# Performance work log

Hardware: AMD Instinct MI355X
Metric: run time of the kernel (lower is better)

Reference implementation:

```python
import jax, jax.numpy as jnp
import numpy as np

SDR_DIM = 65536
HIDDEN = 4096
N_MOD = 2048
PHASE = 2 * N_MOD  # 4096
NORM_EPS = 1e-8


def setup_inputs() -> dict:
    key = jax.random.key(0)
    ks = jax.random.split(key, 12)
    active_sdr = (jax.random.uniform(ks[0], (SDR_DIM,)) < 0.05).astype(jnp.float32)
    velocity = jax.random.normal(ks[1], (2,), dtype=jnp.float32)
    # encoder params (torch Linear: y = x @ W.T + b, W shape (out, in))
    W1 = jax.random.normal(ks[2], (HIDDEN, SDR_DIM), dtype=jnp.float32) * (1.0 / np.sqrt(SDR_DIM))
    b1 = jnp.zeros((HIDDEN,), dtype=jnp.float32)
    W2 = jax.random.normal(ks[3], (PHASE, HIDDEN), dtype=jnp.float32) * (1.0 / np.sqrt(HIDDEN))
    b2 = jnp.zeros((PHASE,), dtype=jnp.float32)
    # velocity encoder (no bias): (n_grid_modules, 2)
    vel_W = jax.random.normal(ks[4], (N_MOD, 2), dtype=jnp.float32) * (1.0 / np.sqrt(2.0))
    # thalamic loop: orthogonal-init square matrices, gain param, hidden state
    def ortho(k, n):
        a = jax.random.normal(k, (n, n), dtype=jnp.float32)
        q, r = jnp.linalg.qr(a)
        return q * jnp.sign(jnp.diag(r))[None, :]
    W_tc = ortho(ks[5], PHASE)
    W_ht = ortho(ks[6], PHASE)
    g_nrt = jnp.ones((PHASE,), dtype=jnp.float32)
    h_tc = jnp.zeros((PHASE,), dtype=jnp.float32)
    return {
        "active_sdr": active_sdr, "velocity": velocity,
        "W1": W1, "b1": b1, "W2": W2, "b2": b2,
        "vel_W": vel_W, "W_tc": W_tc, "W_ht": W_ht,
        "g_nrt": g_nrt, "h_tc": h_tc,
    }


def reference(active_sdr, velocity, W1, b1, W2, b2, vel_W, W_tc, W_ht, g_nrt, h_tc):
    # encoder: Linear -> ReLU -> Linear
    h = jax.nn.relu(W1 @ active_sdr + b1)          # (HIDDEN,)
    z_ego = W2 @ h + b2                            # (PHASE,)
    z = z_ego.reshape(N_MOD, 2)                    # (M, 2)
    # per-module 2D rotation by theta from velocity
    theta = vel_W @ velocity                       # (M,)
    c, s = jnp.cos(theta), jnp.sin(theta)
    x, y = z[:, 0], z[:, 1]
    z_allo = jnp.stack([c * x - s * y, s * x + c * y], axis=-1)  # (M, 2)
    z_flat = z_allo.reshape(PHASE)
    # thalamic loop: h_new = tanh(W_tc z + W_ht h_tc); feedback = sigmoid(g) * h_new
    h_new = jnp.tanh(W_tc @ z_flat + W_ht @ h_tc)
    feedback = jax.nn.sigmoid(g_nrt) * h_new
    z_fb = z_flat + 0.1 * feedback
    # isometry rescale (branchy .item() logic -> jnp.where)
    target_norm = jnp.linalg.norm(z_ego)
    current_norm = jnp.linalg.norm(z_fb)
    rescaled = z_fb * (target_norm / jnp.maximum(current_norm, NORM_EPS))
    out = jnp.where(current_norm > NORM_EPS, rescaled, z_fb)
    out = jnp.where(target_norm > NORM_EPS, out, jnp.zeros_like(z_fb))
    return out
```

## Files before the change

### kernel.cpp

```cpp
#include <hip/hip_runtime.h>
#include <math.h>

#define SDR_DIM 65536
#define HIDDEN  4096
#define NMOD    2048
#define PHASE   4096
#define NGRP_MAX (SDR_DIM / 16)
#define NORM_EPS 1e-8f

__device__ __forceinline__ float waveReduce(float v) {
  #pragma unroll
  for (int off = 32; off > 0; off >>= 1) v += __shfl_down(v, off);
  return v;
}

__global__ __launch_bounds__(1024) void k_compact(const float* __restrict__ sdr,
                                                  unsigned int* __restrict__ packed,
                                                  int* __restrict__ ngrp) {
  __shared__ int wsum[16];
  int t = threadIdx.x;
  int lane = t & 63, wave = t >> 6;

  unsigned int masks[4];
  int cnt = 0;
  const float4* s4 = (const float4*)sdr;
  #pragma unroll
  for (int g = 0; g < 4; ++g) {
    int gid = t * 4 + g;
    unsigned int m = 0;
    #pragma unroll
    for (int q = 0; q < 4; ++q) {
      float4 v = s4[gid * 4 + q];
      m |= (v.x > 0.0f ? 1u : 0u) << (q * 4 + 0);
      m |= (v.y > 0.0f ? 1u : 0u) << (q * 4 + 1);
      m |= (v.z > 0.0f ? 1u : 0u) << (q * 4 + 2);
      m |= (v.w > 0.0f ? 1u : 0u) << (q * 4 + 3);
    }
    masks[g] = m;
    cnt += (m != 0u) ? 1 : 0;
  }

  int inc = cnt;
  #pragma unroll
  for (int d = 1; d < 64; d <<= 1) {
    int v = __shfl_up(inc, d);
    if (lane >= d) inc += v;
  }
  if (lane == 63) wsum[wave] = inc;
  __syncthreads();
  if (t == 0) {
    int s = 0;
    #pragma unroll
    for (int w = 0; w < 16; ++w) { int v = wsum[w]; wsum[w] = s; s += v; }
    *ngrp = s;
  }
  __syncthreads();

  int off = wsum[wave] + (inc - cnt);
  #pragma unroll
  for (int g = 0; g < 4; ++g) {
    if (masks[g]) packed[off++] = (masks[g] << 16) | (unsigned int)(t * 4 + g);
  }
}

__global__ __launch_bounds__(256) void k_h(const float* __restrict__ W1,
                                           const float* __restrict__ b1,
                                           const unsigned int* __restrict__ packed,
                                           const int* __restrict__ ngrpp,
                                           float* __restrict__ h) {
  int lane = threadIdx.x & 63;
  int row = blockIdx.x * 4 + (threadIdx.x >> 6);
  int n = *ngrpp;
  int sub = lane & 3, slot = lane >> 2;
  int shift = 16 + sub * 4;
  const float4* __restrict__ Wr4 = (const float4*)(W1 + (size_t)row * SDR_DIM);

  float acc = 0.0f;
  int k = slot;
  for (; k + 48 < n; k += 64) {
    unsigned int e0 = packed[k];
    unsigned int e1 = packed[k + 16];
    unsigned int e2 = packed[k + 32];
    unsigned int e3 = packed[k + 48];
    float4 f0 = Wr4[(e0 & 0xFFFFu) * 4 + sub];
    float4 f1 = Wr4[(e1 & 0xFFFFu) * 4 + sub];
    float4 f2 = Wr4[(e2 & 0xFFFFu) * 4 + sub];
    float4 f3 = Wr4[(e3 & 0xFFFFu) * 4 + sub];
    unsigned int m0 = (e0 >> shift) & 0xFu;
    unsigned int m1 = (e1 >> shift) & 0xFu;
    unsigned int m2 = (e2 >> shift) & 0xFu;
    unsigned int m3 = (e3 >> shift) & 0xFu;
    acc += (m0 & 1u) ? f0.x : 0.0f; acc += (m0 & 2u) ? f0.y : 0.0f;
    acc += (m0 & 4u) ? f0.z : 0.0f; acc += (m0 & 8u) ? f0.w : 0.0f;
    acc += (m1 & 1u) ? f1.x : 0.0f; acc += (m1 & 2u) ? f1.y : 0.0f;
    acc += (m1 & 4u) ? f1.z : 0.0f; acc += (m1 & 8u) ? f1.w : 0.0f;
    acc += (m2 & 1u) ? f2.x : 0.0f; acc += (m2 & 2u) ? f2.y : 0.0f;
    acc += (m2 & 4u) ? f2.z : 0.0f; acc += (m2 & 8u) ? f2.w : 0.0f;
    acc += (m3 & 1u) ? f3.x : 0.0f; acc += (m3 & 2u) ? f3.y : 0.0f;
    acc += (m3 & 4u) ? f3.z : 0.0f; acc += (m3 & 8u) ? f3.w : 0.0f;
  }
  for (; k < n; k += 16) {
    unsigned int e = packed[k];
    float4 f = Wr4[(e & 0xFFFFu) * 4 + sub];
    unsigned int m = (e >> shift) & 0xFu;
    acc += (m & 1u) ? f.x : 0.0f; acc += (m & 2u) ? f.y : 0.0f;
    acc += (m & 4u) ? f.z : 0.0f; acc += (m & 8u) ? f.w : 0.0f;
  }

  acc = waveReduce(acc);
  if (lane == 0) {
    float v = acc + b1[row];
    h[row] = v > 0.0f ? v : 0.0f;
  }
}

__global__ __launch_bounds__(256) void k_z_rot(const float* __restrict__ W,
                                               const float* __restrict__ x,
                                               const float* __restrict__ b,
                                               const float* __restrict__ velW,
                                               const float* __restrict__ vel,
                                               float* __restrict__ zego,
                                               float* __restrict__ zflat) {
  __shared__ float zs[4];
  int lane = threadIdx.x & 63;
  int wave = threadIdx.x >> 6;
  int row = blockIdx.x * 4 + wave;
  const float4* __restrict__ Wr = (const float4*)(W + (size_t)row * HIDDEN);
  const float4* __restrict__ xv = (const float4*)x;
  float acc = 0.0f;
  #pragma unroll 4
  for (int k = lane; k < HIDDEN / 4; k += 64) {
    float4 w = Wr[k]; float4 v = xv[k];
    acc += w.x * v.x + w.y * v.y + w.z * v.z + w.w * v.w;
  }
  acc = waveReduce(acc);
  if (lane == 0) {
    float v = acc + b[row];
    zego[row] = v;
    zs[wave] = v;
  }
  __syncthreads();
  if (threadIdx.x < 2) {
    int m = blockIdx.x * 2 + threadIdx.x;
    float xx = zs[2 * threadIdx.x];
    float yy = zs[2 * threadIdx.x + 1];
    float th = velW[2 * m] * vel[0] + velW[2 * m + 1] * vel[1];
    float s, c;
    sincosf(th, &s, &c);
    zflat[2 * m]     = c * xx - s * yy;
    zflat[2 * m + 1] = s * xx + c * yy;
  }
}

__global__ __launch_bounds__(256) void k_hnew(const float* __restrict__ Wtc,
                                              const float* __restrict__ Wht,
                                              const float* __restrict__ zflat,
                                              const float* __restrict__ htc,
                                              const float* __restrict__ gnrt,
                                              float* __restrict__ zfb) {
  int lane = threadIdx.x & 63;
  int row = blockIdx.x * 4 + (threadIdx.x >> 6);
  const float4* __restrict__ Ar = (const float4*)(Wtc + (size_t)row * PHASE);
  const float4* __restrict__ Br = (const float4*)(Wht + (size_t)row * PHASE);
  const float4* __restrict__ xv = (const float4*)zflat;
  const float4* __restrict__ hv = (const float4*)htc;
  float acc = 0.0f;
  #pragma unroll 2
  for (int k = lane; k < PHASE / 4; k += 64) {
    float4 a = Ar[k], v = xv[k];
    acc += a.x * v.x + a.y * v.y + a.z * v.z + a.w * v.w;
    float4 bb = Br[k], u = hv[k];
    acc += bb.x * u.x + bb.y * u.y + bb.z * u.z + bb.w * u.w;
  }
  acc = waveReduce(acc);
  if (lane == 0) {
    float hn = tanhf(acc);
    float sg = 1.0f / (1.0f + expf(-gnrt[row]));
    zfb[row] = zflat[row] + 0.1f * sg * hn;
  }
}

__global__ __launch_bounds__(1024) void k_out(const float* __restrict__ zego,
                                              const float* __restrict__ zfb,
                                              float* __restrict__ out) {
  __shared__ float s0[16], s1[16];
  int t = threadIdx.x;
  int lane = t & 63, wave = t >> 6;
  float a = 0.0f, bsum = 0.0f;
  #pragma unroll
  for (int i = 0; i < PHASE / 1024; ++i) {
    float xe = zego[t + i * 1024]; a += xe * xe;
    float xf = zfb[t + i * 1024];  bsum += xf * xf;
  }
  a = waveReduce(a);
  bsum = waveReduce(bsum);
  if (lane == 0) { s0[wave] = a; s1[wave] = bsum; }
  __syncthreads();
  if (t == 0) {
    float ta = 0.0f, tb = 0.0f;
    #pragma unroll
    for (int w = 0; w < 16; ++w) { ta += s0[w]; tb += s1[w]; }
    s0[0] = ta; s1[0] = tb;
  }
  __syncthreads();
  float tn = sqrtf(s0[0]);
  float cn = sqrtf(s1[0]);
  float scale = tn / fmaxf(cn, NORM_EPS);
  #pragma unroll
  for (int i = 0; i < PHASE / 1024; ++i) {
    float v = zfb[t + i * 1024];
    float r = v * scale;
    float o = (cn > NORM_EPS) ? r : v;
    o = (tn > NORM_EPS) ? o : 0.0f;
    out[t + i * 1024] = o;
  }
}

extern "C" void kernel_launch(void* const* d_in, const int* in_sizes, int n_in,
                              void* d_out, int out_size, void* d_ws, size_t ws_size,
                              hipStream_t stream) {
  const float* sdr  = (const float*)d_in[0];
  const float* vel  = (const float*)d_in[1];
  const float* W1   = (const float*)d_in[2];
  const float* b1   = (const float*)d_in[3];
  const float* W2   = (const float*)d_in[4];
  const float* b2   = (const float*)d_in[5];
  const float* velW = (const float*)d_in[6];
  const float* Wtc  = (const float*)d_in[7];
  const float* Wht  = (const float*)d_in[8];
  const float* gnrt = (const float*)d_in[9];
  const float* htc  = (const float*)d_in[10];
  float* out = (float*)d_out;

  char* ws = (char*)d_ws;
  int* ngrp = (int*)ws;
  unsigned int* packed = (unsigned int*)(ws + 64);
  float* h     = (float*)(ws + 64 + NGRP_MAX * sizeof(unsigned int));
  float* zego  = h + HIDDEN;
  float* zflat = zego + PHASE;
  float* zfb   = zflat + PHASE;

  k_compact<<<1, 1024, 0, stream>>>(sdr, packed, ngrp);
  k_h<<<HIDDEN / 4, 256, 0, stream>>>(W1, b1, packed, ngrp, h);
  k_z_rot<<<PHASE / 4, 256, 0, stream>>>(W2, h, b2, velW, vel, zego, zflat);
  k_hnew<<<PHASE / 4, 256, 0, stream>>>(Wtc, Wht, zflat, htc, gnrt, zfb);
  k_out<<<1, 1024, 0, stream>>>(zego, zfb, out);
}
```

Measured before the change: 218.1 us.

## Skip zero h_tc GEMV, parallelize mask building, use nontemporal weight loads

Adds a device-side check whether h_tc is all zero and skips the W_ht matrix-vector product in that case, avoiding a full pass over a large weight matrix. Splits SDR mask construction into a multi-block kernel before the single-block prefix/emit kernel. Switches weight streams to nontemporal loads and deepens the gather unroll in the sparse first layer. Adds an extra launch and a flag read in exchange.

```diff
diff --git a/kernel.cpp b/kernel.cpp
--- a/kernel.cpp
+++ b/kernel.cpp
@@ -5,8 +5,10 @@
 #define HIDDEN  4096
 #define NMOD    2048
 #define PHASE   4096
-#define NGRP_MAX (SDR_DIM / 16)
+#define NGRP    (SDR_DIM / 16)
 #define NORM_EPS 1e-8f
+
+typedef float fx4 __attribute__((ext_vector_type(4)));
 
 __device__ __forceinline__ float waveReduce(float v) {
   #pragma unroll
@@ -14,32 +16,50 @@
   return v;
 }
 
-__global__ __launch_bounds__(1024) void k_compact(const float* __restrict__ sdr,
-                                                  unsigned int* __restrict__ packed,
-                                                  int* __restrict__ ngrp) {
+__device__ __forceinline__ fx4 ntload4(const fx4* p) {
+  return __builtin_nontemporal_load(p);
+}
+
+__global__ __launch_bounds__(256) void k_masks(const float* __restrict__ sdr,
+                                               unsigned int* __restrict__ masks) {
+  int g = blockIdx.x * 256 + threadIdx.x;
+  const fx4* s4 = (const fx4*)sdr;
+  unsigned int m = 0;
+  #pragma unroll
+  for (int q = 0; q < 4; ++q) {
+    fx4 v = s4[g * 4 + q];
+    m |= (v.x > 0.0f ? 1u : 0u) << (q * 4 + 0);
+    m |= (v.y > 0.0f ? 1u : 0u) << (q * 4 + 1);
+    m |= (v.z > 0.0f ? 1u : 0u) << (q * 4 + 2);
+    m |= (v.w > 0.0f ? 1u : 0u) << (q * 4 + 3);
+  }
+  masks[g] = m;
+}
+
+__global__ __launch_bounds__(1024) void k_emit(const unsigned int* __restrict__ masks,
+                                               const float* __restrict__ htc,
+                                               unsigned int* __restrict__ packed,
+                                               int* __restrict__ ngrp,
+                                               int* __restrict__ ntc) {
   __shared__ int wsum[16];
+  __shared__ int sflag;
   int t = threadIdx.x;
   int lane = t & 63, wave = t >> 6;
-
-  unsigned int masks[4];
+  if (t == 0) sflag = 0;
+  __syncthreads();
+
+  bool nz = false;
+  #pragma unroll
+  for (int i = 0; i < PHASE / 1024; ++i) nz |= (htc[t + i * 1024] != 0.0f);
+  if (nz) sflag = 1;
+
+  unsigned int m[4];
   int cnt = 0;
-  const float4* s4 = (const float4*)sdr;
   #pragma unroll
   for (int g = 0; g < 4; ++g) {
-    int gid = t * 4 + g;
-    unsigned int m = 0;
-    #pragma unroll
-    for (int q = 0; q < 4; ++q) {
-      float4 v = s4[gid * 4 + q];
-      m |= (v.x > 0.0f ? 1u : 0u) << (q * 4 + 0);
-      m |= (v.y > 0.0f ? 1u : 0u) << (q * 4 + 1);
-      m |= (v.z > 0.0f ? 1u : 0u) << (q * 4 + 2);
-      m |= (v.w > 0.0f ? 1u : 0u) << (q * 4 + 3);
-    }
-    masks[g] = m;
-    cnt += (m != 0u) ? 1 : 0;
-  }
-
+    m[g] = masks[t * 4 + g];
+    cnt += (m[g] != 0u) ? 1 : 0;
+  }
   int inc = cnt;
   #pragma unroll
   for (int d = 1; d < 64; d <<= 1) {
@@ -53,13 +73,13 @@
     #pragma unroll
     for (int w = 0; w < 16; ++w) { int v = wsum[w]; wsum[w] = s; s += v; }
     *ngrp = s;
-  }
-  __syncthreads();
-
+    *ntc = sflag;
+  }
+  __syncthreads();
   int off = wsum[wave] + (inc - cnt);
   #pragma unroll
   for (int g = 0; g < 4; ++g) {
-    if (masks[g]) packed[off++] = (masks[g] << 16) | (unsigned int)(t * 4 + g);
+    if (m[g]) packed[off++] = (m[g] << 16) | (unsigned int)(t * 4 + g);
   }
 }
 
@@ -73,38 +93,34 @@
   int n = *ngrpp;
   int sub = lane & 3, slot = lane >> 2;
   int shift = 16 + sub * 4;
-  const float4* __restrict__ Wr4 = (const float4*)(W1 + (size_t)row * SDR_DIM);
+  const fx4* __restrict__ Wr4 = (const fx4*)(W1 + (size_t)row * SDR_DIM);
 
   float acc = 0.0f;
   int k = slot;
-  for (; k + 48 < n; k += 64) {
-    unsigned int e0 = packed[k];
-    unsigned int e1 = packed[k + 16];
-    unsigned int e2 = packed[k + 32];
-    unsigned int e3 = packed[k + 48];
-    float4 f0 = Wr4[(e0 & 0xFFFFu) * 4 + sub];
-    float4 f1 = Wr4[(e1 & 0xFFFFu) * 4 + sub];
-    float4 f2 = Wr4[(e2 & 0xFFFFu) * 4 + sub];
-    float4 f3 = Wr4[(e3 & 0xFFFFu) * 4 + sub];
-    unsigned int m0 = (e0 >> shift) & 0xFu;
-    unsigned int m1 = (e1 >> shift) & 0xFu;
-    unsigned int m2 = (e2 >> shift) & 0xFu;
-    unsigned int m3 = (e3 >> shift) & 0xFu;
-    acc += (m0 & 1u) ? f0.x : 0.0f; acc += (m0 & 2u) ? f0.y : 0.0f;
-    acc += (m0 & 4u) ? f0.z : 0.0f; acc += (m0 & 8u) ? f0.w : 0.0f;
-    acc += (m1 & 1u) ? f1.x : 0.0f; acc += (m1 & 2u) ? f1.y : 0.0f;
-    acc += (m1 & 4u) ? f1.z : 0.0f; acc += (m1 & 8u) ? f1.w : 0.0f;
-    acc += (m2 & 1u) ? f2.x : 0.0f; acc += (m2 & 2u) ? f2.y : 0.0f;
-    acc += (m2 & 4u) ? f2.z : 0.0f; acc += (m2 & 8u) ? f2.w : 0.0f;
-    acc += (m3 & 1u) ? f3.x : 0.0f; acc += (m3 & 2u) ? f3.y : 0.0f;
-    acc += (m3 & 4u) ? f3.z : 0.0f; acc += (m3 & 8u) ? f3.w : 0.0f;
+  for (; k + 112 < n; k += 128) {
+    unsigned int e[8];
+    fx4 f[8];
+    #pragma unroll
+    for (int j = 0; j < 8; ++j) e[j] = packed[k + 16 * j];
+    #pragma unroll
+    for (int j = 0; j < 8; ++j) f[j] = ntload4(Wr4 + ((e[j] & 0xFFFFu) * 4 + sub));
+    #pragma unroll
+    for (int j = 0; j < 8; ++j) {
+      unsigned int mj = (e[j] >> shift) & 0xFu;
+      acc += (mj & 1u) ? f[j].x : 0.0f;
+      acc += (mj & 2u) ? f[j].y : 0.0f;
+      acc += (mj & 4u) ? f[j].z : 0.0f;
+      acc += (mj & 8u) ? f[j].w : 0.0f;
+    }
   }
   for (; k < n; k += 16) {
     unsigned int e = packed[k];
-    float4 f = Wr4[(e & 0xFFFFu) * 4 + sub];
-    unsigned int m = (e >> shift) & 0xFu;
-    acc += (m & 1u) ? f.x : 0.0f; acc += (m & 2u) ? f.y : 0.0f;
-    acc += (m & 4u) ? f.z : 0.0f; acc += (m & 8u) ? f.w : 0.0f;
+    fx4 f = ntload4(Wr4 + ((e & 0xFFFFu) * 4 + sub));
+    unsigned int mj = (e >> shift) & 0xFu;
+    acc += (mj & 1u) ? f.x : 0.0f;
+    acc += (mj & 2u) ? f.y : 0.0f;
+    acc += (mj & 4u) ? f.z : 0.0f;
+    acc += (mj & 8u) ? f.w : 0.0f;
   }
 
   acc = waveReduce(acc);
@@ -125,12 +141,12 @@
   int lane = threadIdx.x & 63;
   int wave = threadIdx.x >> 6;
   int row = blockIdx.x * 4 + wave;
-  const float4* __restrict__ Wr = (const float4*)(W + (size_t)row * HIDDEN);
-  const float4* __restrict__ xv = (const float4*)x;
+  const fx4* __restrict__ Wr = (const fx4*)(W + (size_t)row * HIDDEN);
+  const fx4* __restrict__ xv = (const fx4*)x;
   float acc = 0.0f;
   #pragma unroll 4
   for (int k = lane; k < HIDDEN / 4; k += 64) {
-    float4 w = Wr[k]; float4 v = xv[k];
+    fx4 w = ntload4(Wr + k); fx4 v = xv[k];
     acc += w.x * v.x + w.y * v.y + w.z * v.z + w.w * v.w;
   }
   acc = waveReduce(acc);
@@ -157,20 +173,26 @@
                                               const float* __restrict__ zflat,
                                               const float* __restrict__ htc,
                                               const float* __restrict__ gnrt,
+                                              const int* __restrict__ ntc,
                                               float* __restrict__ zfb) {
   int lane = threadIdx.x & 63;
   int row = blockIdx.x * 4 + (threadIdx.x >> 6);
-  const float4* __restrict__ Ar = (const float4*)(Wtc + (size_t)row * PHASE);
-  const float4* __restrict__ Br = (const float4*)(Wht + (size_t)row * PHASE);
-  const float4* __restrict__ xv = (const float4*)zflat;
-  const float4* __restrict__ hv = (const float4*)htc;
+  const fx4* __restrict__ Ar = (const fx4*)(Wtc + (size_t)row * PHASE);
+  const fx4* __restrict__ xv = (const fx4*)zflat;
   float acc = 0.0f;
-  #pragma unroll 2
+  #pragma unroll 4
   for (int k = lane; k < PHASE / 4; k += 64) {
-    float4 a = Ar[k], v = xv[k];
+    fx4 a = ntload4(Ar + k); fx4 v = xv[k];
     acc += a.x * v.x + a.y * v.y + a.z * v.z + a.w * v.w;
-    float4 bb = Br[k], u = hv[k];
-    acc += bb.x * u.x + bb.y * u.y + bb.z * u.z + bb.w * u.w;
+  }
+  if (*ntc) {
+    const fx4* __restrict__ Br = (const fx4*)(Wht + (size_t)row * PHASE);
+    const fx4* __restrict__ hv = (const fx4*)htc;
+    #pragma unroll 4
+    for (int k = lane; k < PHASE / 4; k += 64) {
+      fx4 bb = ntload4(Br + k); fx4 u = hv[k];
+      acc += bb.x * u.x + bb.y * u.y + bb.z * u.z + bb.w * u.w;
+    }
   }
   acc = waveReduce(acc);
   if (lane == 0) {
@@ -233,16 +255,19 @@
   float* out = (float*)d_out;
 
   char* ws = (char*)d_ws;
-  int* ngrp = (int*)ws;
-  unsigned int* packed = (unsigned int*)(ws + 64);
-  float* h     = (float*)(ws + 64 + NGRP_MAX * sizeof(unsigned int));
+  unsigned int* masks  = (unsigned int*)ws;
+  int*          ngrp   = (int*)(ws + 16384);
+  int*          ntc    = (int*)(ws + 16384 + 64);
+  unsigned int* packed = (unsigned int*)(ws + 16384 + 128);
+  float* h     = (float*)(ws + 32768 + 256);
   float* zego  = h + HIDDEN;
   float* zflat = zego + PHASE;
   float* zfb   = zflat + PHASE;
 
-  k_compact<<<1, 1024, 0, stream>>>(sdr, packed, ngrp);
+  k_masks<<<NGRP / 256, 256, 0, stream>>>(sdr, masks);
+  k_emit<<<1, 1024, 0, stream>>>(masks, htc, packed, ngrp, ntc);
   k_h<<<HIDDEN / 4, 256, 0, stream>>>(W1, b1, packed, ngrp, h);
   k_z_rot<<<PHASE / 4, 256, 0, stream>>>(W2, h, b2, velW, vel, zego, zflat);
-  k_hnew<<<PHASE / 4, 256, 0, stream>>>(Wtc, Wht, zflat, htc, gnrt, zfb);
+  k_hnew<<<PHASE / 4, 256, 0, stream>>>(Wtc, Wht, zflat, htc, gnrt, ntc, zfb);
   k_out<<<1, 1024, 0, stream>>>(zego, zfb, out);
 }
```

After: 176.5 us, median of 2. 1.24x faster.
